# Performance work log

Hardware: AMD Instinct MI355X
Metric: run time of the kernel (lower is better)

The kernel has to match this reference:

```python
import jax, jax.numpy as jnp
import numpy as np

B, N, D, H = 2048, 100, 512, 8
TANH_C = 10.0


def setup_inputs() -> dict:
    key = jax.random.key(0)
    ks = jax.random.split(key, 16)
    s = 1.0 / np.sqrt(D)
    inp = {
        "node_embeddings": jax.random.normal(ks[0], (B, N, D), jnp.float32),
        "graph_embedding": jax.random.normal(ks[1], (B, D), jnp.float32),
        "target_idx": jax.random.randint(ks[2], (B,), 0, N, jnp.int32),
        "mask": jax.random.randint(ks[3], (B, N), 0, 2, jnp.int32),
    }
    for i, name in enumerate(["W_target", "W_global", "W_K1", "W_K2", "W_Q", "W_V",
                              "Wq_mha", "Wk_mha", "Wv_mha", "Wo_mha"]):
        inp[name] = jax.random.normal(ks[4 + i], (D, D), jnp.float32) * s
    return inp


def reference(node_embeddings, graph_embedding, target_idx, mask,
              W_target, W_global, W_K1, W_K2, W_Q, W_V,
              Wq_mha, Wk_mha, Wv_mha, Wo_mha):
    # one pointer-network decode step (Decoder loop body)
    b, n, d = node_embeddings.shape
    dh = d // H
    scale_h = 1.0 / (dh ** 0.5)

    # target_embeddings = node_embeddings[arange(B), env.target_stack]
    tgt = jnp.take_along_axis(node_embeddings, target_idx[:, None, None].astype(jnp.int32), axis=1)[:, 0, :]  # [B,D]

    # context = W_target(tgt) + W_global(graph)   (nn.Linear: x @ W.T)
    context = (tgt @ W_target.T + graph_embedding @ W_global.T)[:, None, :]  # [B,1,D]
    node_keys = node_embeddings @ W_K1.T   # [B,N,D]
    node_vals = node_embeddings @ W_V.T    # [B,N,D]

    # MultiHeadAttention([context, keys, values]) with internal per-head projections
    q = (context @ Wq_mha.T).reshape(b, 1, H, dh)
    k = (node_keys @ Wk_mha.T).reshape(b, n, H, dh)
    v = (node_vals @ Wv_mha.T).reshape(b, n, H, dh)
    scores = jnp.einsum("bqhd,bnhd->bhqn", q, k) * scale_h   # [B,H,1,N]
    attn = jax.nn.softmax(scores, axis=-1)
    mha = jnp.einsum("bhqn,bnhd->bqhd", attn, v).reshape(b, 1, d) @ Wo_mha.T  # [B,1,D]

    query = mha @ W_Q.T                    # [B,1,D]
    key2 = node_embeddings @ W_K2.T        # [B,N,D]

    # logits = (query @ key2^T) / sqrt(D), tanh-clipped, masked
    logits = jnp.einsum("bqd,bnd->bqn", query, key2)[:, 0, :] / (d ** 0.5)  # [B,N]
    logits = TANH_C * jnp.tanh(logits)
    logits = logits - mask.astype(logits.dtype) * 1e9
    log_p = jax.nn.log_softmax(logits, axis=1)  # [B,N]
    return log_p
```

## Files before the change

kernel.cpp:

```cpp
#include <hip/hip_runtime.h>

#define DD 512
#define NNODE 100
#define NH 8

typedef __attribute__((ext_vector_type(4))) float f32x4;
typedef __attribute__((ext_vector_type(8))) short s16x8;

__device__ __forceinline__ unsigned short f2bf(float x) {
  union { float f; unsigned int u; } v; v.f = x;
  unsigned int r = v.u + 0x7fffu + ((v.u >> 16) & 1u);
  return (unsigned short)(r >> 16);
}
__device__ __forceinline__ float bf2f(unsigned short u) {
  union { unsigned int u; float f; } v; v.u = ((unsigned int)u) << 16;
  return v.f;
}

__device__ __forceinline__ void gemm_accum(
    f32x4 acc[2][2], const float* __restrict__ A, const float* __restrict__ B,
    const int* __restrict__ gidx, int gmul, int K, int lda, int ldb,
    int transB, int m0, int n0,
    unsigned short (*As)[40], unsigned short (*Bs)[40])
{
  const int t = threadIdx.x;
  const int wid = t >> 6, lane = t & 63;
  const int wr = wid >> 1, wc = wid & 1;
  const int r16 = lane & 15, kg = (lane >> 4) * 8;
  const int tr = t >> 3, kq = t & 7;
  const int bn = t & 63, bk = t >> 6;

  for (int k0 = 0; k0 < K; k0 += 32) {
#pragma unroll
    for (int rp = 0; rp < 2; ++rp) {
      const int row = tr + rp * 32;
      const int gi = m0 + row;
      long ab = (long)gi * lda;
      if (gidx) ab += (long)gidx[gi] * gmul;
      const float4 av = *(const float4*)(A + ab + k0 + kq * 4);
      unsigned int p0 = (unsigned)f2bf(av.x) | ((unsigned)f2bf(av.y) << 16);
      unsigned int p1 = (unsigned)f2bf(av.z) | ((unsigned)f2bf(av.w) << 16);
      *(uint2*)(&As[row][kq * 4]) = make_uint2(p0, p1);
    }
    if (transB) {
#pragma unroll
      for (int rp = 0; rp < 2; ++rp) {
        const int row = tr + rp * 32;
        const float4 bv = *(const float4*)(B + (long)(n0 + row) * ldb + k0 + kq * 4);
        unsigned int p0 = (unsigned)f2bf(bv.x) | ((unsigned)f2bf(bv.y) << 16);
        unsigned int p1 = (unsigned)f2bf(bv.z) | ((unsigned)f2bf(bv.w) << 16);
        *(uint2*)(&Bs[row][kq * 4]) = make_uint2(p0, p1);
      }
    } else {
#pragma unroll
      for (int pp = 0; pp < 8; ++pp) {
        const int k = bk + pp * 4;
        Bs[bn][k] = f2bf(B[(long)(k0 + k) * ldb + n0 + bn]);
      }
    }
    __syncthreads();
    s16x8 a0 = *(const s16x8*)(&As[wr * 32 + r16][kg]);
    s16x8 a1 = *(const s16x8*)(&As[wr * 32 + 16 + r16][kg]);
    s16x8 b0 = *(const s16x8*)(&Bs[wc * 32 + r16][kg]);
    s16x8 b1 = *(const s16x8*)(&Bs[wc * 32 + 16 + r16][kg]);
    acc[0][0] = __builtin_amdgcn_mfma_f32_16x16x32_bf16(a0, b0, acc[0][0], 0, 0, 0);
    acc[0][1] = __builtin_amdgcn_mfma_f32_16x16x32_bf16(a0, b1, acc[0][1], 0, 0, 0);
    acc[1][0] = __builtin_amdgcn_mfma_f32_16x16x32_bf16(a1, b0, acc[1][0], 0, 0, 0);
    acc[1][1] = __builtin_amdgcn_mfma_f32_16x16x32_bf16(a1, b1, acc[1][1], 0, 0, 0);
    __syncthreads();
  }
}

__device__ __forceinline__ void gemm_epilogue(
    f32x4 acc[2][2], void* Cv, int ldc, float alpha, float beta, int obf16,
    int m0, int n0)
{
  const int t = threadIdx.x;
  const int wid = t >> 6, lane = t & 63;
  const int wr = wid >> 1, wc = wid & 1;
  const int r16 = lane & 15;
#pragma unroll
  for (int si = 0; si < 2; ++si)
#pragma unroll
    for (int sj = 0; sj < 2; ++sj)
#pragma unroll
      for (int r = 0; r < 4; ++r) {
        const int row = m0 + wr * 32 + si * 16 + (lane >> 4) * 4 + r;
        const int col = n0 + wc * 32 + sj * 16 + r16;
        const long ci = (long)row * ldc + col;
        float v = alpha * acc[si][sj][r];
        if (obf16) {
          ((unsigned short*)Cv)[ci] = f2bf(v);
        } else {
          float* C = (float*)Cv;
          if (beta != 0.f) v = fmaf(beta, C[ci], v);
          C[ci] = v;
        }
      }
}

__global__ __launch_bounds__(256) void gemm_mfma(
    const float* __restrict__ A, const float* __restrict__ B, void* Cv,
    int K, int lda, int ldb, int ldc,
    long aoffz, long boffz, long coffz,
    int transB, float alpha, float beta, int obf16)
{
  __shared__ unsigned short As[64][40];
  __shared__ unsigned short Bs[64][40];
  A += (long)blockIdx.z * aoffz;
  B += (long)blockIdx.z * boffz;
  f32x4 acc[2][2] = {};
  gemm_accum(acc, A, B, nullptr, 0, K, lda, ldb, transB,
             blockIdx.y * 64, blockIdx.x * 64, As, Bs);
  void* Cz = obf16 ? (void*)((unsigned short*)Cv + (long)blockIdx.z * coffz)
                   : (void*)((float*)Cv + (long)blockIdx.z * coffz);
  gemm_epilogue(acc, Cz, ldc, alpha, beta, obf16, blockIdx.y * 64, blockIdx.x * 64);
}

struct Fold5Args {
  const float* A[5]; const float* B[5]; float* C[5]; float al[5];
};

__global__ __launch_bounds__(256) void fold5_kernel(Fold5Args fa) {
  __shared__ unsigned short As[64][40];
  __shared__ unsigned short Bs[64][40];
  const int z = blockIdx.z;
  f32x4 acc[2][2] = {};
  gemm_accum(acc, fa.A[z], fa.B[z], nullptr, 0, 512, 512, 512, 0,
             blockIdx.y * 64, blockIdx.x * 64, As, Bs);
  gemm_epilogue(acc, fa.C[z], 512, fa.al[z], 0.f, 0, blockIdx.y * 64, blockIdx.x * 64);
}

__global__ __launch_bounds__(256) void qbuf_kernel(
    const float* __restrict__ node, const float* __restrict__ graph,
    const int* __restrict__ tidx, const float* __restrict__ A1,
    const float* __restrict__ A2, float* __restrict__ C)
{
  __shared__ unsigned short As[64][40];
  __shared__ unsigned short Bs[64][40];
  f32x4 acc[2][2] = {};
  gemm_accum(acc, node, A1, tidx, DD, DD, NNODE * DD, DD, 1,
             blockIdx.y * 64, blockIdx.x * 64, As, Bs);
  __syncthreads();
  gemm_accum(acc, graph, A2, nullptr, 0, DD, DD, DD, 1,
             blockIdx.y * 64, blockIdx.x * 64, As, Bs);
  gemm_epilogue(acc, C, DD, 1.f, 0.f, 0, blockIdx.y * 64, blockIdx.x * 64);
}

__global__ __launch_bounds__(256) void attn_fused(
    const float* __restrict__ node, const unsigned short* __restrict__ qk16,
    unsigned short* __restrict__ nb16, float* __restrict__ ctx)
{
  const int b = blockIdx.x;
  const int t = threadIdx.x;
  const int lane = t & 63;
  const int wid = t >> 6;
  const int r16 = lane & 15;
  const int rg = lane >> 4;

  __shared__ unsigned short nf[16 * 512];
  __shared__ unsigned short qf[16 * 512];
  __shared__ float Pl[4][16][8];
  __shared__ float rfl[4][8];

  {
    const unsigned short* qb = qk16 + (long)b * (NH * DD);
    for (int slot = t; slot < 1024; slot += 256) {
      const int s = slot >> 6, vl = slot & 63;
      const int h = vl & 15, g = vl >> 4;
      s16x8 v = {0, 0, 0, 0, 0, 0, 0, 0};
      if (h < NH) v = *(const s16x8*)(qb + h * DD + s * 32 + g * 8);
      *(s16x8*)(&qf[slot * 8]) = v;
    }
  }

  const int r0 = t >> 7;
  const int c4 = (t * 4) & 511;
  const int s_c = c4 >> 5, rg_c = (c4 >> 3) & 3, j_c = c4 & 7;
  const int slotbase = (s_c * 4 + rg_c) * 16 + r0;
  const int d0 = t * 2;
  const int cbase = ((d0 >> 5) * 4 + ((d0 >> 3) & 3)) * 128 + (d0 & 7);
  const int fb = (rg * 16 + r16) * 8;

  const float* nbase = node + (long)b * (NNODE * DD);
  float4 rs[8];
  {
    const int lim = NNODE * DD;
#pragma unroll
    for (int i = 0; i < 8; ++i) {
      const int e = 4 * t + 1024 * i;
      rs[i] = (e < lim) ? *(const float4*)(nbase + e) : make_float4(0.f, 0.f, 0.f, 0.f);
    }
  }

  float m = -3.0e38f, l = 0.f;
  float2 c2[NH];
#pragma unroll
  for (int h = 0; h < NH; ++h) { c2[h].x = 0.f; c2[h].y = 0.f; }

  for (int c = 0; c < 7; ++c) {
    const int c0 = c * 16;
    __syncthreads();
#pragma unroll
    for (int i = 0; i < 8; ++i) {
      ushort4 h4;
      h4.x = f2bf(rs[i].x); h4.y = f2bf(rs[i].y);
      h4.z = f2bf(rs[i].z); h4.w = f2bf(rs[i].w);
      *(ushort4*)(&nf[(slotbase + 2 * i) * 8 + j_c]) = h4;
      const int row = r0 + 2 * i;
      if (c0 + row < NNODE)
        *(ushort4*)(nb16 + ((long)b * NNODE + c0 + row) * DD + c4) = h4;
    }
    if (c < 6) {
      const int nc0 = c0 + 16;
      const int lim = (NNODE - nc0) * DD;
#pragma unroll
      for (int i = 0; i < 8; ++i) {
        const int e = 4 * t + 1024 * i;
        rs[i] = (e < lim) ? *(const float4*)(nbase + (long)nc0 * DD + e)
                          : make_float4(0.f, 0.f, 0.f, 0.f);
      }
    }
    __syncthreads();

    f32x4 acc = {0.f, 0.f, 0.f, 0.f};
#pragma unroll
    for (int s = 0; s < 16; ++s) {
      const s16x8 av = *(const s16x8*)(&nf[s * 512 + fb]);
      const s16x8 bv = *(const s16x8*)(&qf[s * 512 + fb]);
      acc = __builtin_amdgcn_mfma_f32_16x16x32_bf16(av, bv, acc, 0, 0, 0);
    }
#pragma unroll
    for (int r = 0; r < 4; ++r)
      if (c0 + rg * 4 + r >= NNODE) acc[r] = -3.0e38f;

    float cm = fmaxf(fmaxf(acc[0], acc[1]), fmaxf(acc[2], acc[3]));
    cm = fmaxf(cm, __shfl_xor(cm, 16));
    cm = fmaxf(cm, __shfl_xor(cm, 32));
    const float mn = fmaxf(m, cm);
    const float rf = __expf(m - mn);
    float p[4], ps = 0.f;
#pragma unroll
    for (int r = 0; r < 4; ++r) { p[r] = __expf(acc[r] - mn); ps += p[r]; }
    ps += __shfl_xor(ps, 16);
    ps += __shfl_xor(ps, 32);
    l = l * rf + ps;
    m = mn;
    if (r16 < NH) {
#pragma unroll
      for (int r = 0; r < 4; ++r) Pl[wid][rg * 4 + r][r16] = p[r];
      if (rg == 0) rfl[wid][r16] = rf;
    }
    asm volatile("s_waitcnt lgkmcnt(0)" ::: "memory");

    {
      const f32x4 rf0 = *(const f32x4*)(&rfl[wid][0]);
      const f32x4 rf1 = *(const f32x4*)(&rfl[wid][4]);
#pragma unroll
      for (int h = 0; h < 4; ++h) { c2[h].x *= rf0[h]; c2[h].y *= rf0[h]; }
#pragma unroll
      for (int h = 0; h < 4; ++h) { c2[4 + h].x *= rf1[h]; c2[4 + h].y *= rf1[h]; }
#pragma unroll
      for (int n = 0; n < 16; ++n) {
        const unsigned int nv = *(const unsigned int*)(&nf[cbase + n * 8]);
        const float x0 = bf2f((unsigned short)(nv & 0xffffu));
        const float x1 = bf2f((unsigned short)(nv >> 16));
        const f32x4 p0 = *(const f32x4*)(&Pl[wid][n][0]);
        const f32x4 p1 = *(const f32x4*)(&Pl[wid][n][4]);
#pragma unroll
        for (int h = 0; h < 4; ++h) {
          c2[h].x = fmaf(p0[h], x0, c2[h].x);
          c2[h].y = fmaf(p0[h], x1, c2[h].y);
          c2[4 + h].x = fmaf(p1[h], x0, c2[4 + h].x);
          c2[4 + h].y = fmaf(p1[h], x1, c2[4 + h].y);
        }
      }
    }
  }

  if (r16 < NH && rg == 0) rfl[wid][r16] = 1.f / l;
  asm volatile("s_waitcnt lgkmcnt(0)" ::: "memory");
  {
    const f32x4 i0 = *(const f32x4*)(&rfl[wid][0]);
    const f32x4 i1 = *(const f32x4*)(&rfl[wid][4]);
    float* cb = ctx + (long)b * (NH * DD) + d0;
#pragma unroll
    for (int h = 0; h < 4; ++h) {
      cb[h * DD] = c2[h].x * i0[h];
      cb[h * DD + 1] = c2[h].y * i0[h];
      cb[(4 + h) * DD] = c2[4 + h].x * i1[h];
      cb[(4 + h) * DD + 1] = c2[4 + h].y * i1[h];
    }
  }
}

__global__ __launch_bounds__(128) void logits_kernel(
    const unsigned short* __restrict__ nb16, const unsigned short* __restrict__ qk216,
    const int* __restrict__ mask, float* __restrict__ out)
{
  const int b = blockIdx.x;
  const int t = threadIdx.x;
  const int wid = t >> 6, lane = t & 63;
  const int r16 = lane & 15, rg = lane >> 4;
  __shared__ float sl[112];
  const unsigned short* qb = qk216 + (long)b * DD + rg * 8;

  for (int ti = wid; ti < 7; ti += 2) {
    const int arow = min(ti * 16 + r16, NNODE - 1);
    const unsigned short* ap = nb16 + ((long)b * NNODE + arow) * DD + rg * 8;
    f32x4 acc = {0.f, 0.f, 0.f, 0.f};
#pragma unroll
    for (int s = 0; s < 16; ++s) {
      const s16x8 av = *(const s16x8*)(ap + s * 32);
      const s16x8 bv = *(const s16x8*)(qb + s * 32);
      acc = __builtin_amdgcn_mfma_f32_16x16x32_bf16(av, bv, acc, 0, 0, 0);
    }
    if (r16 == 0) {
#pragma unroll
      for (int r = 0; r < 4; ++r) {
        const int n = ti * 16 + rg * 4 + r;
        if (n < 112) sl[n] = acc[r];
      }
    }
  }
  __syncthreads();
  if (t < 64) {
    float v0 = -3.0e38f, v1 = -3.0e38f;
    if (lane < NNODE)
      v0 = 10.f * tanhf(sl[lane]) - (float)mask[b * NNODE + lane] * 1e9f;
    if (lane + 64 < NNODE)
      v1 = 10.f * tanhf(sl[lane + 64]) - (float)mask[b * NNODE + lane + 64] * 1e9f;
    float mx = fmaxf(v0, v1);
#pragma unroll
    for (int off = 1; off < 64; off <<= 1) mx = fmaxf(mx, __shfl_xor(mx, off));
    float e = 0.f;
    if (lane < NNODE) e += __expf(v0 - mx);
    if (lane + 64 < NNODE) e += __expf(v1 - mx);
#pragma unroll
    for (int off = 1; off < 64; off <<= 1) e += __shfl_xor(e, off);
    const float lse = mx + __logf(e);
    float* ob = out + (long)b * NNODE;
    if (lane < NNODE) ob[lane] = v0 - lse;
    if (lane + 64 < NNODE) ob[lane + 64] = v1 - lse;
  }
}

extern "C" void kernel_launch(void* const* d_in, const int* in_sizes, int n_in,
                              void* d_out, int out_size, void* d_ws, size_t ws_size,
                              hipStream_t stream) {
  const float* node     = (const float*)d_in[0];
  const float* graph    = (const float*)d_in[1];
  const int*   tidx     = (const int*)d_in[2];
  const int*   mask     = (const int*)d_in[3];
  const float* W_target = (const float*)d_in[4];
  const float* W_global = (const float*)d_in[5];
  const float* W_K1     = (const float*)d_in[6];
  const float* W_K2     = (const float*)d_in[7];
  const float* W_Q      = (const float*)d_in[8];
  const float* W_V      = (const float*)d_in[9];
  const float* Wq_mha   = (const float*)d_in[10];
  const float* Wk_mha   = (const float*)d_in[11];
  const float* Wv_mha   = (const float*)d_in[12];
  const float* Wo_mha   = (const float*)d_in[13];
  float* out = (float*)d_out;

  float* base = (float*)d_ws;
  unsigned short* nb16 = (unsigned short*)base;
  long off = 2048L * NNODE * DD / 2;
  float* A1 = base + off;        off += 262144;
  float* A2 = base + off;        off += 262144;
  float* Wkc = base + off;       off += 262144;
  float* Wvc = base + off;       off += 262144;
  float* Woq = base + off;       off += 262144;
  float* qbuf = base + off;      off += 2048L * 512;
  unsigned short* qk16 = (unsigned short*)(base + off);  off += 2048L * 4096 / 2;
  float* ctxb = base + off;      off += 2048L * 4096;
  float* preo = base + off;      off += 2048L * 512;
  float* query = base + off;     off += 2048L * 512;
  unsigned short* qk216 = (unsigned short*)(base + off); off += 2048L * 512 / 2;

  dim3 blk(256);
  const float SH = 0.125f;
  const float SD = 0.044194173824f;

  Fold5Args fa;
  fa.A[0] = Wq_mha;  fa.B[0] = W_target; fa.C[0] = A1;  fa.al[0] = 1.f;
  fa.A[1] = Wq_mha;  fa.B[1] = W_global; fa.C[1] = A2;  fa.al[1] = 1.f;
  fa.A[2] = Wk_mha;  fa.B[2] = W_K1;     fa.C[2] = Wkc; fa.al[2] = SH;
  fa.A[3] = Wv_mha;  fa.B[3] = W_V;      fa.C[3] = Wvc; fa.al[3] = 1.f;
  fa.A[4] = W_Q;     fa.B[4] = Wo_mha;   fa.C[4] = Woq; fa.al[4] = 1.f;
  fold5_kernel<<<dim3(8, 8, 5), blk, 0, stream>>>(fa);
  qbuf_kernel<<<dim3(8, 32), blk, 0, stream>>>(node, graph, tidx, A1, A2, qbuf);
  gemm_mfma<<<dim3(8, 32, 8), blk, 0, stream>>>(qbuf, Wkc, qk16,
      64, 512, 512, 4096, 64, 32768, 512, 0, 1.f, 0.f, 1);
  attn_fused<<<dim3(2048), dim3(256), 0, stream>>>(node, qk16, nb16, ctxb);
  gemm_mfma<<<dim3(1, 32, 8), blk, 0, stream>>>(ctxb, Wvc, preo,
      512, 4096, 512, 512, 512, 32768, 64, 1, 1.f, 0.f, 0);
  gemm_mfma<<<dim3(8, 32, 1), blk, 0, stream>>>(preo, Woq, query,
      512, 512, 512, 512, 0, 0, 0, 1, 1.f, 0.f, 0);
  gemm_mfma<<<dim3(8, 32, 1), blk, 0, stream>>>(query, W_K2, qk216,
      512, 512, 512, 512, 0, 0, 0, 0, SD, 0.f, 1);
  logits_kernel<<<dim3(2048), dim3(128), 0, stream>>>(nb16, qk216, mask, out);

  (void)in_sizes; (void)n_in; (void)out_size; (void)ws_size;
}
```

Measured before the change: 340.2 us.

## Double-buffer node tile in LDS with XOR swizzle and shrink query staging

The attention kernel now double-buffers the bf16 node tile in shared memory, dropping one barrier per chunk. It writes the tile with an XOR-swizzled slot layout to cut bank conflicts, and delays the global bf16 stores until after the next prefetch is issued. The query staging buffer is compacted to only the 8 real heads with padding, and the B operand is zeroed in registers instead. The logits kernel now launches 256 threads so four waves share the seven row tiles; the extra LDS and index math add some register and occupancy pressure.

Result: no change. 338.8 us (-0.4%).

```diff
diff --git a/kernel.cpp b/kernel.cpp
--- a/kernel.cpp
+++ b/kernel.cpp
@@ -158,29 +158,32 @@
   const int r16 = lane & 15;
   const int rg = lane >> 4;
 
-  __shared__ unsigned short nf[16 * 512];
-  __shared__ unsigned short qf[16 * 512];
+  __shared__ unsigned short nf[2][16 * 512];
+  __shared__ unsigned short qf[16 * 288];
   __shared__ float Pl[4][16][8];
   __shared__ float rfl[4][8];
 
   {
     const unsigned short* qb = qk16 + (long)b * (NH * DD);
-    for (int slot = t; slot < 1024; slot += 256) {
-      const int s = slot >> 6, vl = slot & 63;
-      const int h = vl & 15, g = vl >> 4;
-      s16x8 v = {0, 0, 0, 0, 0, 0, 0, 0};
-      if (h < NH) v = *(const s16x8*)(qb + h * DD + s * 32 + g * 8);
-      *(s16x8*)(&qf[slot * 8]) = v;
+    for (int slot = t; slot < 512; slot += 256) {
+      const int s = slot >> 5;
+      const int idx = slot & 31;
+      const int h = idx >> 2, g = idx & 3;
+      *(s16x8*)(&qf[s * 288 + idx * 8 + (idx >> 3) * 8]) =
+          *(const s16x8*)(qb + h * DD + s * 32 + g * 8);
     }
   }
 
   const int r0 = t >> 7;
   const int c4 = (t * 4) & 511;
-  const int s_c = c4 >> 5, rg_c = (c4 >> 3) & 3, j_c = c4 & 7;
-  const int slotbase = (s_c * 4 + rg_c) * 16 + r0;
+  const int slotbase = ((c4 >> 3) * 16) + r0;
+  const int j_c = c4 & 7;
   const int d0 = t * 2;
-  const int cbase = ((d0 >> 5) * 4 + ((d0 >> 3) & 3)) * 128 + (d0 & 7);
-  const int fb = (rg * 16 + r16) * 8;
+  const int cslot0 = (d0 >> 3) * 16;
+  const int cxor = (d0 >> 3) & 7;
+  const int cj = d0 & 7;
+  const int qidx = (r16 & 7) * 4 + rg;
+  const int qfb = qidx * 8 + (qidx >> 3) * 8;
 
   const float* nbase = node + (long)b * (NNODE * DD);
   float4 rs[8];
@@ -197,20 +200,22 @@
   float2 c2[NH];
 #pragma unroll
   for (int h = 0; h < NH; ++h) { c2[h].x = 0.f; c2[h].y = 0.f; }
+  ushort4 h4s[8];
 
   for (int c = 0; c < 7; ++c) {
     const int c0 = c * 16;
-    __syncthreads();
+    const int cur = c & 1;
 #pragma unroll
     for (int i = 0; i < 8; ++i) {
       ushort4 h4;
       h4.x = f2bf(rs[i].x); h4.y = f2bf(rs[i].y);
       h4.z = f2bf(rs[i].z); h4.w = f2bf(rs[i].w);
-      *(ushort4*)(&nf[(slotbase + 2 * i) * 8 + j_c]) = h4;
-      const int row = r0 + 2 * i;
-      if (c0 + row < NNODE)
-        *(ushort4*)(nb16 + ((long)b * NNODE + c0 + row) * DD + c4) = h4;
-    }
+      h4s[i] = h4;
+      const int slot = slotbase + 2 * i;
+      const int phys = slot ^ ((slot >> 4) & 7);
+      *(ushort4*)(&nf[cur][phys * 8 + j_c]) = h4;
+    }
+    __syncthreads();
     if (c < 6) {
       const int nc0 = c0 + 16;
       const int lim = (NNODE - nc0) * DD;
@@ -221,13 +226,20 @@
                           : make_float4(0.f, 0.f, 0.f, 0.f);
       }
     }
-    __syncthreads();
+#pragma unroll
+    for (int i = 0; i < 8; ++i) {
+      const int row = r0 + 2 * i;
+      if (c0 + row < NNODE)
+        *(ushort4*)(nb16 + ((long)b * NNODE + c0 + row) * DD + c4) = h4s[i];
+    }
 
     f32x4 acc = {0.f, 0.f, 0.f, 0.f};
 #pragma unroll
     for (int s = 0; s < 16; ++s) {
-      const s16x8 av = *(const s16x8*)(&nf[s * 512 + fb]);
-      const s16x8 bv = *(const s16x8*)(&qf[s * 512 + fb]);
+      const int slr = (s * 4 + rg) * 16 + r16;
+      const s16x8 av = *(const s16x8*)(&nf[cur][(slr ^ ((s * 4 + rg) & 7)) * 8]);
+      s16x8 bv = {0, 0, 0, 0, 0, 0, 0, 0};
+      if (r16 < NH) bv = *(const s16x8*)(&qf[s * 288 + qfb]);
       acc = __builtin_amdgcn_mfma_f32_16x16x32_bf16(av, bv, acc, 0, 0, 0);
     }
 #pragma unroll
@@ -262,7 +274,8 @@
       for (int h = 0; h < 4; ++h) { c2[4 + h].x *= rf1[h]; c2[4 + h].y *= rf1[h]; }
 #pragma unroll
       for (int n = 0; n < 16; ++n) {
-        const unsigned int nv = *(const unsigned int*)(&nf[cbase + n * 8]);
+        const int cphys = (cslot0 + n) ^ cxor;
+        const unsigned int nv = *(const unsigned int*)(&nf[cur][cphys * 8 + cj]);
         const float x0 = bf2f((unsigned short)(nv & 0xffffu));
         const float x1 = bf2f((unsigned short)(nv >> 16));
         const f32x4 p0 = *(const f32x4*)(&Pl[wid][n][0]);
@@ -294,7 +307,7 @@
   }
 }
 
-__global__ __launch_bounds__(128) void logits_kernel(
+__global__ __launch_bounds__(256) void logits_kernel(
     const unsigned short* __restrict__ nb16, const unsigned short* __restrict__ qk216,
     const int* __restrict__ mask, float* __restrict__ out)
 {
@@ -305,7 +318,7 @@
   __shared__ float sl[112];
   const unsigned short* qb = qk216 + (long)b * DD + rg * 8;
 
-  for (int ti = wid; ti < 7; ti += 2) {
+  for (int ti = wid; ti < 7; ti += 4) {
     const int arow = min(ti * 16 + r16, NNODE - 1);
     const unsigned short* ap = nb16 + ((long)b * NNODE + arow) * DD + rg * 8;
     f32x4 acc = {0.f, 0.f, 0.f, 0.f};
@@ -400,7 +413,7 @@
       512, 512, 512, 512, 0, 0, 0, 1, 1.f, 0.f, 0);
   gemm_mfma<<<dim3(8, 32, 1), blk, 0, stream>>>(query, W_K2, qk216,
       512, 512, 512, 512, 0, 0, 0, 0, SD, 0.f, 1);
-  logits_kernel<<<dim3(2048), dim3(128), 0, stream>>>(nb16, qk216, mask, out);
+  logits_kernel<<<dim3(2048), blk, 0, stream>>>(nb16, qk216, mask, out);
 
   (void)in_sizes; (void)n_in; (void)out_size; (void)ws_size;
 }
```
